# Kernel tuning notes

Hardware: AMD Instinct MI355X
Metric: run time of the kernel (lower is better)

Reference implementation:

```python
import jax, jax.numpy as jnp
import numpy as np

N_EMBD = 1024
N_HEAD = 16
B, T = 2, 2048
EPS_LN = 1e-5
EPS_RENORM = 1e-8


def _layernorm(x, w, b):
    mu = jnp.mean(x, axis=-1, keepdims=True)
    var = jnp.mean(jnp.square(x - mu), axis=-1, keepdims=True)
    return (x - mu) * jax.lax.rsqrt(var + EPS_LN) * w + b


def setup_inputs() -> dict:
    key = jax.random.key(0)
    ks = jax.random.split(key, 8)
    C = N_EMBD
    s = 0.02
    return {
        "x": jax.random.normal(ks[0], (B, T, C), jnp.float32),
        "ln1_w": jnp.ones((C,), jnp.float32),
        "ln1_b": jnp.zeros((C,), jnp.float32),
        "w_attn": jax.random.normal(ks[1], (C, 3 * C), jnp.float32) * s,
        "b_attn": jnp.zeros((3 * C,), jnp.float32),
        "w_attn_proj": jax.random.normal(ks[2], (C, C), jnp.float32) * s,
        "b_attn_proj": jnp.zeros((C,), jnp.float32),
        "threshold": jnp.full((N_HEAD,), 0.01, jnp.float32),
        "leak": jnp.full((N_HEAD,), 2.0, jnp.float32),
        "steepness": jnp.full((N_HEAD,), 2.0, jnp.float32),
        "ln2_w": jnp.ones((C,), jnp.float32),
        "ln2_b": jnp.zeros((C,), jnp.float32),
        "w_fc": jax.random.normal(ks[3], (C, 4 * C), jnp.float32) * s,
        "b_fc": jnp.zeros((4 * C,), jnp.float32),
        "w_mlp_proj": jax.random.normal(ks[4], (4 * C, C), jnp.float32) * s,
        "b_mlp_proj": jnp.zeros((C,), jnp.float32),
    }


def _ember_block(x, ln1_w, ln1_b, w_attn, b_attn, w_attn_proj, b_attn_proj,
                 threshold, leak, steepness, ln2_w, ln2_b,
                 w_fc, b_fc, w_mlp_proj, b_mlp_proj):
    Bx, Tx, C = x.shape
    H = N_HEAD
    D = C // H

    h = _layernorm(x, ln1_w, ln1_b)
    qkv = h @ w_attn + b_attn                      # [B,T,3C]
    q, k, v = jnp.split(qkv, 3, axis=-1)
    q = q.reshape(Bx, Tx, H, D).transpose(0, 2, 1, 3)  # [B,H,T,D]
    k = k.reshape(Bx, Tx, H, D).transpose(0, 2, 1, 3)
    v = v.reshape(Bx, Tx, H, D).transpose(0, 2, 1, 3)

    att = jnp.einsum('bhqd,bhkd->bhqk', q, k) * (1.0 / np.sqrt(D))
    causal = jnp.tril(jnp.ones((Tx, Tx), bool))
    att = jnp.where(causal[None, None], att, -jnp.inf)
    p = jax.nn.softmax(att, axis=-1)               # [B,H,T,T]

    # per-head LIF gating
    th = (jnp.abs(threshold) * 0.1)[None, :, None, None]
    lk = jax.nn.sigmoid(leak)[None, :, None, None]
    st = jax.nn.softplus(steepness)[None, :, None, None]
    fire = jax.nn.sigmoid(st * (p - th))
    w = fire + lk * (1.0 - fire)
    m = p * w
    m = m / (jnp.sum(m, axis=-1, keepdims=True) + EPS_RENORM)

    y = jnp.einsum('bhqk,bhkd->bhqd', m, v)
    y = y.transpose(0, 2, 1, 3).reshape(Bx, Tx, C)
    y = y @ w_attn_proj + b_attn_proj
    x = x + y

    h2 = _layernorm(x, ln2_w, ln2_b)
    h2 = jax.nn.gelu(h2 @ w_fc + b_fc, approximate=False)
    x = x + (h2 @ w_mlp_proj + b_mlp_proj)
    return x


def reference(x, ln1_w, ln1_b, w_attn, b_attn, w_attn_proj, b_attn_proj,
              threshold, leak, steepness, ln2_w, ln2_b,
              w_fc, b_fc, w_mlp_proj, b_mlp_proj):
    return _ember_block(x, ln1_w, ln1_b, w_attn, b_attn, w_attn_proj, b_attn_proj,
                        threshold, leak, steepness, ln2_w, ln2_b,
                        w_fc, b_fc, w_mlp_proj, b_mlp_proj)
```

## Files before the change

kernel.cpp:

```cpp
#include <hip/hip_runtime.h>
#include <hip/hip_bf16.h>
#include <math.h>

typedef __bf16 bf16_t;
typedef __bf16 bf16x8 __attribute__((ext_vector_type(8)));
typedef __bf16 bf16x4 __attribute__((ext_vector_type(4)));
typedef float  f32x4  __attribute__((ext_vector_type(4)));
typedef unsigned int u32;

static constexpr int C_    = 1024;
static constexpr int NH    = 16;
static constexpr int DH    = 64;
static constexpr int BB    = 2;
static constexpr int TT    = 2048;
static constexpr int MROWS = BB * TT;
static constexpr float LOG2E = 1.4426950408889634f;

__device__ __forceinline__ void gload_lds16(const bf16_t* src, bf16_t* dst) {
  __builtin_amdgcn_global_load_lds(
      (const __attribute__((address_space(1))) u32*)(src),
      (__attribute__((address_space(3))) u32*)(dst),
      16, 0, 0);
}

__device__ __forceinline__ u32 cvt_pk_bf16(float a, float b) {
  u32 r;
  asm("v_cvt_pk_bf16_f32 %0, %1, %2" : "=v"(r) : "v"(a), "v"(b));
  return r;
}

__device__ __forceinline__ float fexp2(float x) {
#if __has_builtin(__builtin_amdgcn_exp2f)
  return __builtin_amdgcn_exp2f(x);
#else
  return exp2f(x);
#endif
}
__device__ __forceinline__ float frcp(float x) {
#if __has_builtin(__builtin_amdgcn_rcpf)
  return __builtin_amdgcn_rcpf(x);
#else
  return 1.0f / x;
#endif
}

__device__ __forceinline__ int sc_to_t(int s, int c) {
  if (s < 32)  return s;
  if (s < 64)  return 32 + (s - 32) * 2 + c;
  if (s < 96)  return 96 + (s - 64) * 3 + c;
  return 192 + (s - 96) * 4 + c;
}

__device__ __forceinline__ void item64_to_uc(int item, int& u, int& c) {
  if (item < 8)       { u = item;               c = 0; }
  else if (item < 24) { int v = item - 8;  u = 8  + (v >> 1); c = v & 1; }
  else if (item < 48) { int v = item - 24; u = 16 + v / 3;    c = v - 3 * (v / 3); }
  else                { int v = item - 48; u = 24 + (v >> 2); c = v & 3; }
}

__global__ __launch_bounds__(256) void ln_bf16(
    const float* __restrict__ x, const float* __restrict__ w,
    const float* __restrict__ b, bf16_t* __restrict__ out)
{
  const int row = blockIdx.x;
  const int tid = threadIdx.x;
  const float4 v = reinterpret_cast<const float4*>(x + (size_t)row * C_)[tid];
  float s  = v.x + v.y + v.z + v.w;
  float s2 = v.x*v.x + v.y*v.y + v.z*v.z + v.w*v.w;
#pragma unroll
  for (int m = 1; m < 64; m <<= 1) { s += __shfl_xor(s, m); s2 += __shfl_xor(s2, m); }
  __shared__ float red[8];
  const int wv = tid >> 6;
  if ((tid & 63) == 0) { red[wv] = s; red[4 + wv] = s2; }
  __syncthreads();
  s  = red[0] + red[1] + red[2] + red[3];
  s2 = red[4] + red[5] + red[6] + red[7];
  const float mu   = s * (1.0f / C_);
  const float rstd = rsqrtf(s2 * (1.0f / C_) - mu * mu + 1e-5f);
  const float4 wv4 = reinterpret_cast<const float4*>(w)[tid];
  const float4 bv4 = reinterpret_cast<const float4*>(b)[tid];
  bf16x4 o;
  o[0] = (bf16_t)((v.x - mu) * rstd * wv4.x + bv4.x);
  o[1] = (bf16_t)((v.y - mu) * rstd * wv4.y + bv4.y);
  o[2] = (bf16_t)((v.z - mu) * rstd * wv4.z + bv4.z);
  o[3] = (bf16_t)((v.w - mu) * rstd * wv4.w + bv4.w);
  *reinterpret_cast<bf16x4*>(out + (size_t)row * C_ + tid * 4) = o;
}

__global__ __launch_bounds__(256) void transpose_w(
    const float* __restrict__ in, bf16_t* __restrict__ out, int K, int N)
{
  __shared__ float tile[32][33];
  const int tx = threadIdx.x & 31, ty = threadIdx.x >> 5;
  const int n0 = blockIdx.x * 32, k0 = blockIdx.y * 32;
#pragma unroll
  for (int i = 0; i < 4; ++i)
    tile[ty + i * 8][tx] = in[(size_t)(k0 + ty + i * 8) * N + n0 + tx];
  __syncthreads();
#pragma unroll
  for (int i = 0; i < 4; ++i)
    out[(size_t)(n0 + ty + i * 8) * K + k0 + tx] = (bf16_t)tile[tx][ty + i * 8];
}

__global__ __launch_bounds__(256) void transpose_v(
    const bf16_t* __restrict__ in, bf16_t* __restrict__ out)
{
  __shared__ bf16_t tile[32][33];
  const int bh = blockIdx.z;
  const bf16_t* src = in  + (size_t)bh * TT * DH;
  bf16_t*       dst = out + (size_t)bh * TT * DH;
  const int tx = threadIdx.x & 31, ty = threadIdx.x >> 5;
  const int t0 = blockIdx.x * 32, d0 = blockIdx.y * 32;
#pragma unroll
  for (int i = 0; i < 4; ++i)
    tile[ty + i * 8][tx] = src[(size_t)(t0 + ty + i * 8) * DH + d0 + tx];
  __syncthreads();
#pragma unroll
  for (int i = 0; i < 4; ++i)
    dst[(size_t)(d0 + ty + i * 8) * TT + t0 + tx] = tile[tx][ty + i * 8];
}

template<int EPI>
__global__ __launch_bounds__(256) void gemm_bf16(
    const bf16_t* __restrict__ A, const bf16_t* __restrict__ Bt,
    const float* __restrict__ bias, const float* __restrict__ resid,
    float* __restrict__ fout, bf16_t* __restrict__ bout0,
    bf16_t* __restrict__ bout1, bf16_t* __restrict__ bout2,
    int M, int N, int K)
{
  constexpr int BM = 128, BN = 128, BK = 64;
  __shared__ bf16_t As[BM * BK];
  __shared__ bf16_t Bs[BN * BK];
  const int tid  = threadIdx.x;
  const int wave = tid >> 6, lane = tid & 63;
  const int r = lane & 15, g = lane >> 4;
  const int wm = wave >> 1, wn = wave & 1;
  const int bm = blockIdx.x, bn = blockIdx.y;

  const bf16_t* Abase = A  + (size_t)bm * BM * K;
  const bf16_t* Bbase = Bt + (size_t)bn * BN * K;

  f32x4 acc[4][4] = {};

  for (int kt = 0; kt < K; kt += BK) {
#pragma unroll
    for (int it = 0; it < 4; ++it) {
      const int c0 = it * 256 + wave * 64;
      const int idx = c0 + lane;
      const int rr = idx >> 3, cc = idx & 7;
      const int gs = cc ^ (rr & 7);
      gload_lds16(Abase + (size_t)rr * K + kt + gs * 8, As + c0 * 8);
    }
#pragma unroll
    for (int it = 0; it < 4; ++it) {
      const int c0 = it * 256 + wave * 64;
      const int idx = c0 + lane;
      const int rr = idx >> 3, cc = idx & 7;
      const int gs = cc ^ (rr & 7);
      gload_lds16(Bbase + (size_t)rr * K + kt + gs * 8, Bs + c0 * 8);
    }
    asm volatile("s_waitcnt vmcnt(0)" ::: "memory");
    __syncthreads();
#pragma unroll
    for (int s = 0; s < 2; ++s) {
      bf16x8 af[4], bfr[4];
#pragma unroll
      for (int mi = 0; mi < 4; ++mi) {
        const int rr = wm * 64 + mi * 16 + r;
        const int ch = (s * 4 + g) ^ (rr & 7);
        af[mi] = *reinterpret_cast<const bf16x8*>(&As[rr * BK + ch * 8]);
      }
#pragma unroll
      for (int ni = 0; ni < 4; ++ni) {
        const int rr = wn * 64 + ni * 16 + r;
        const int ch = (s * 4 + g) ^ (rr & 7);
        bfr[ni] = *reinterpret_cast<const bf16x8*>(&Bs[rr * BK + ch * 8]);
      }
#pragma unroll
      for (int mi = 0; mi < 4; ++mi)
#pragma unroll
        for (int ni = 0; ni < 4; ++ni)
          acc[mi][ni] = __builtin_amdgcn_mfma_f32_16x16x32_bf16(
              af[mi], bfr[ni], acc[mi][ni], 0, 0, 0);
    }
    __syncthreads();
  }

#pragma unroll
  for (int mi = 0; mi < 4; ++mi) {
#pragma unroll
    for (int ni = 0; ni < 4; ++ni) {
      const int grow0 = bm * BM + wm * 64 + mi * 16 + g * 4;
      const int gcol  = bn * BN + wn * 64 + ni * 16 + r;
      const float bv = bias[gcol];
#pragma unroll
      for (int i = 0; i < 4; ++i) {
        const int grow = grow0 + i;
        float v = acc[mi][ni][i] + bv;
        if constexpr (EPI == 0) {
          const int which = gcol >> 10;
          const int c0 = gcol & 1023;
          const int hh = c0 >> 6, dd = c0 & 63;
          const int bb = grow >> 11, t = grow & 2047;
          bf16_t* dst = (which == 0) ? bout0 : (which == 1) ? bout1 : bout2;
          dst[((size_t)(bb * NH + hh) * TT + t) * DH + dd] = (bf16_t)v;
        } else if constexpr (EPI == 1) {
          const size_t o = (size_t)grow * N + gcol;
          fout[o] = v + resid[o];
        } else {
          const float gl = 0.5f * v * (1.0f + erff(v * 0.70710678118654752f));
          bout0[(size_t)grow * N + gcol] = (bf16_t)gl;
        }
      }
    }
  }
}


__global__ __launch_bounds__(256, 4) void attn_p1(
    const bf16_t* __restrict__ Q, const bf16_t* __restrict__ Km,
    float2* __restrict__ mzP)
{
  __shared__ bf16_t Ks[2][64 * 64];
  const int tid = threadIdx.x;
  const int w = tid >> 6, lane = tid & 63;
  const int r = lane & 15, g = lane >> 4;
  const int bid = blockIdx.x;
  const int bh  = (bid & 7) * 4 + ((bid >> 3) & 3);
  int u, c; item64_to_uc(bid >> 5, u, c);
  const int cmax = u >> 3;
  const bool diag = (c == cmax);
  const int nt = diag ? (u & 7) + 1 : 8;
  const int s = 4 * u + w;
  const int row0 = u * 64 + w * 16;
  const int qrow = row0 + r;

  const bf16_t* Qh = Q  + (size_t)bh * TT * DH;
  const bf16_t* Kh = Km + (size_t)bh * TT * DH;
  const float SCL = 0.125f * LOG2E;

  bf16x8 qf[2];
#pragma unroll
  for (int s2 = 0; s2 < 2; ++s2) {
    bf16x8 t = *reinterpret_cast<const bf16x8*>(Qh + (size_t)qrow * DH + s2 * 32 + g * 8);
#pragma unroll
    for (int i = 0; i < 8; ++i) t[i] = (bf16_t)((float)t[i] * SCL);
    qf[s2] = t;
  }

  auto STAGEK = [&](int b, int t8) {
#pragma unroll
    for (int it = 0; it < 2; ++it) {
      const int idx = it * 256 + tid;
      const int rr = idx >> 3, cc = idx & 7, gs = cc ^ (rr & 7);
      gload_lds16(Kh + (size_t)(c * 512 + t8 * 64 + rr) * DH + gs * 8, &Ks[b][idx * 8]);
    }
  };

  float runM = -1e30f, runZ = 0.f;
  STAGEK(0, 0);
  for (int t8 = 0; t8 < nt; ++t8) {
    const int b = t8 & 1;
    asm volatile("s_waitcnt vmcnt(0)" ::: "memory");
    __syncthreads();
    if (t8 + 1 < nt) STAGEK(b ^ 1, t8 + 1);
    f32x4 sfT[4] = {};
#pragma unroll
    for (int s2 = 0; s2 < 2; ++s2) {
      bf16x8 kf[4];
#pragma unroll
      for (int ni = 0; ni < 4; ++ni)
        kf[ni] = *reinterpret_cast<const bf16x8*>(
            &Ks[b][(ni * 16 + r) * 64 + (((s2 << 2) | g) ^ (r & 7)) * 8]);
#pragma unroll
      for (int ni = 0; ni < 4; ++ni)
        sfT[ni] = __builtin_amdgcn_mfma_f32_16x16x32_bf16(kf[ni], qf[s2], sfT[ni], 0, 0, 0);
    }
    const bool dm = diag && (t8 == nt - 1);
    const int kbase = c * 512 + t8 * 64;
    float xv[16];
#pragma unroll
    for (int ni = 0; ni < 4; ++ni)
#pragma unroll
      for (int j = 0; j < 4; ++j) {
        float x = sfT[ni][j];
        if (dm) {
          const int kcol = kbase + ni * 16 + g * 4 + j;
          if (kcol > qrow) x = -1e30f;
        }
        xv[ni * 4 + j] = x;
      }
    float nm = runM;
#pragma unroll
    for (int e = 0; e < 16; ++e) nm = fmaxf(nm, xv[e]);
    float z = runZ * fexp2(runM - nm);
#pragma unroll
    for (int e = 0; e < 16; ++e) z += fexp2(xv[e] - nm);
    runM = nm; runZ = z;
  }
#pragma unroll
  for (int msk = 16; msk < 64; msk <<= 1) {
    const float om = __shfl_xor(runM, msk), oz = __shfl_xor(runZ, msk);
    const float nm = fmaxf(runM, om);
    runZ = runZ * fexp2(runM - nm) + oz * fexp2(om - nm);
    runM = nm;
  }
  if (lane < 16)
    mzP[((size_t)(bh * 128 + s) * 4 + c) * 16 + r] = make_float2(runM, runZ);
}

__global__ __launch_bounds__(256, 4) void attn_p3(
    const bf16_t* __restrict__ Q, const bf16_t* __restrict__ Km,
    const bf16_t* __restrict__ Vt, const float2* __restrict__ mzP,
    bf16_t* __restrict__ Y, uint2* __restrict__ yaccA,
    uint2* __restrict__ yaccB, float* __restrict__ denP,
    const float* __restrict__ thrp, const float* __restrict__ leakp,
    const float* __restrict__ steepp)
{
  __shared__ bf16_t Ks[2][64 * 64];
  __shared__ bf16_t Vs[2][64 * 64];
  __shared__ __align__(16) u32 Ms[4][512];

  const int tid = threadIdx.x;
  const int w = tid >> 6, lane = tid & 63;
  const int r = lane & 15, g = lane >> 4;
  const int bid = blockIdx.x;
  const int bh  = (bid & 7) * 4 + ((bid >> 3) & 3);
  int u, c; item64_to_uc(bid >> 5, u, c);
  const int cmax = u >> 3;
  const bool diag = (c == cmax);
  const int nt = diag ? (u & 7) + 1 : 8;
  const int nch = cmax + 1;
  const int s = 4 * u + w;
  const int row0 = u * 64 + w * 16;
  const int qrow = row0 + r;
  const int hh = bh & (NH - 1), bb = bh >> 4;

  const bf16_t* Qh  = Q  + (size_t)bh * TT * DH;
  const bf16_t* Kh  = Km + (size_t)bh * TT * DH;
  const bf16_t* Vth = Vt + (size_t)bh * TT * DH;

  const float lk  = 1.0f / (1.0f + expf(-leakp[hh]));
  const float ilk = 1.0f - lk;
  const float st  = log1pf(expf(steepp[hh]));
  const float Lst = LOG2E * st;
  const float A0  = Lst * (fabsf(thrp[hh]) * 0.1f);

  float M = -1e30f, Z = 0.f;
  for (int c2 = 0; c2 < nch; ++c2) {
    const float2 mz = mzP[((size_t)(bh * 128 + s) * 4 + c2) * 16 + r];
    const float nm = fmaxf(M, mz.x);
    Z = Z * fexp2(M - nm) + mz.y * fexp2(mz.x - nm);
    M = nm;
  }
  const float rcpZ = frcp(Z);

  const float SCL = 0.125f * LOG2E;
  bf16x8 qf[2];
#pragma unroll
  for (int s2 = 0; s2 < 2; ++s2) {
    bf16x8 t = *reinterpret_cast<const bf16x8*>(Qh + (size_t)qrow * DH + s2 * 32 + g * 8);
#pragma unroll
    for (int i = 0; i < 8; ++i) t[i] = (bf16_t)((float)t[i] * SCL);
    qf[s2] = t;
  }
  bf16x8 ones;
#pragma unroll
  for (int i = 0; i < 8; ++i) ones[i] = (bf16_t)1.0f;

  uint2* MsU2 = reinterpret_cast<uint2*>(&Ms[w][0]);
  uint4* MsU4 = reinterpret_cast<uint4*>(&Ms[w][0]);

  auto STAGE = [&](int b, int t8) {
    const int kbase = c * 512 + t8 * 64;
#pragma unroll
    for (int it = 0; it < 2; ++it) {
      const int idx = it * 256 + tid;
      const int rr = idx >> 3, cc = idx & 7, gs = cc ^ (rr & 7);
      gload_lds16(Kh + (size_t)(kbase + rr) * DH + gs * 8, &Ks[b][idx * 8]);
      gload_lds16(Vth + (size_t)rr * TT + kbase + gs * 8, &Vs[b][idx * 8]);
    }
  };

  f32x4 yacc[4] = {};
  f32x4 dacc = {};

  STAGE(0, 0);
  for (int t8 = 0; t8 < nt; ++t8) {
    const int b = t8 & 1;
    asm volatile("s_waitcnt vmcnt(0)" ::: "memory");
    __syncthreads();
    if (t8 + 1 < nt) STAGE(b ^ 1, t8 + 1);
    const int kbase = c * 512 + t8 * 64;
    f32x4 sfT[4] = {};
#pragma unroll
    for (int s2 = 0; s2 < 2; ++s2) {
      bf16x8 kf[4];
#pragma unroll
      for (int ni = 0; ni < 4; ++ni)
        kf[ni] = *reinterpret_cast<const bf16x8*>(
            &Ks[b][(ni * 16 + r) * 64 + (((s2 << 2) | g) ^ (r & 7)) * 8]);
#pragma unroll
      for (int ni = 0; ni < 4; ++ni)
        sfT[ni] = __builtin_amdgcn_mfma_f32_16x16x32_bf16(kf[ni], qf[s2], sfT[ni], 0, 0, 0);
    }
    const bool dm = diag && (t8 == nt - 1);
#pragma unroll
    for (int ni = 0; ni < 4; ++ni) {
      float mv[4];
#pragma unroll
      for (int j = 0; j < 4; ++j) {
        float x = sfT[ni][j];
        if (dm) {
          const int kcol = kbase + ni * 16 + g * 4 + j;
          if (kcol > qrow) x = -1e30f;
        }
        const float p    = fexp2(x - M) * rcpZ;
        const float fire = frcp(1.0f + fexp2(A0 - Lst * p));
        mv[j] = p * fmaf(ilk, fire, lk);
      }
      MsU2[r * 16 + ((4 * ni + g) ^ ((r & 7) << 1))] =
          make_uint2(cvt_pk_bf16(mv[0], mv[1]), cvt_pk_bf16(mv[2], mv[3]));
    }
#pragma unroll
    for (int s2 = 0; s2 < 2; ++s2) {
      const uint4 aw = MsU4[r * 8 + ((s2 * 4 + g) ^ (r & 7))];
      const bf16x8 af = __builtin_bit_cast(bf16x8, aw);
      bf16x8 vf[4];
#pragma unroll
      for (int ni = 0; ni < 4; ++ni)
        vf[ni] = *reinterpret_cast<const bf16x8*>(
            &Vs[b][(ni * 16 + r) * 64 + (((s2 << 2) | g) ^ (r & 7)) * 8]);
#pragma unroll
      for (int ni = 0; ni < 4; ++ni)
        yacc[ni] = __builtin_amdgcn_mfma_f32_16x16x32_bf16(af, vf[ni], yacc[ni], 0, 0, 0);
      dacc = __builtin_amdgcn_mfma_f32_16x16x32_bf16(af, ones, dacc, 0, 0, 0);
    }
  }

  if (nch == 1) {
#pragma unroll
    for (int j = 0; j < 4; ++j) {
      const float rd = frcp(dacc[j] + 1e-8f);
      const int t = row0 + g * 4 + j;
#pragma unroll
      for (int ni = 0; ni < 4; ++ni)
        Y[((size_t)(bb * TT + t)) * C_ + hh * DH + ni * 16 + r] =
            (bf16_t)(yacc[ni][j] * rd);
    }
  } else {
    const int pid = bh * 288 + (sc_to_t(s, c) - 32);
    uint2* pb = (pid < 4096) ? (yaccA + (size_t)pid * 256)
                             : (yaccB + (size_t)(pid - 4096) * 256);
#pragma unroll
    for (int ni = 0; ni < 4; ++ni)
      pb[ni * 64 + lane] =
          make_uint2(cvt_pk_bf16(yacc[ni][0], yacc[ni][1]),
                     cvt_pk_bf16(yacc[ni][2], yacc[ni][3]));
    if (r == 0)
      *reinterpret_cast<float4*>(&denP[(size_t)pid * 16 + g * 4]) =
          make_float4(dacc[0], dacc[1], dacc[2], dacc[3]);
  }
}

__global__ __launch_bounds__(256) void attn_p4(
    const uint2* __restrict__ yaccA, const uint2* __restrict__ yaccB,
    const float* __restrict__ denP, bf16_t* __restrict__ Y)
{
  const int bid = blockIdx.x;
  const int bh  = bid / 96;
  const int s   = 32 + (bid - bh * 96);
  const int nch = (s >> 5) + 1;
  const int hh = bh & (NH - 1), bb = bh >> 4;

  const int tid = threadIdx.x;
  const int w = tid >> 6, lane = tid & 63;
  const int r = lane & 15, g = lane >> 4;

  float acc[4] = {};
  float den[4] = {};
  for (int c = 0; c < nch; ++c) {
    const int pid = bh * 288 + (sc_to_t(s, c) - 32);
    const uint2* pb = (pid < 4096) ? (yaccA + (size_t)pid * 256)
                                   : (yaccB + (size_t)(pid - 4096) * 256);
    const uint2 u = pb[w * 64 + lane];
    acc[0] += __builtin_bit_cast(float, (u.x & 0xFFFFu) << 16);
    acc[1] += __builtin_bit_cast(float, (u.x & 0xFFFF0000u));
    acc[2] += __builtin_bit_cast(float, (u.y & 0xFFFFu) << 16);
    acc[3] += __builtin_bit_cast(float, (u.y & 0xFFFF0000u));
    const float4 d4 = *reinterpret_cast<const float4*>(&denP[(size_t)pid * 16 + g * 4]);
    den[0] += d4.x; den[1] += d4.y; den[2] += d4.z; den[3] += d4.w;
  }
#pragma unroll
  for (int j = 0; j < 4; ++j) {
    const float rd = 1.0f / (den[j] + 1e-8f);
    const int t = s * 16 + g * 4 + j;
    Y[((size_t)(bb * TT + t)) * C_ + hh * DH + w * 16 + r] = (bf16_t)(acc[j] * rd);
  }
}

extern "C" void kernel_launch(void* const* d_in, const int* in_sizes, int n_in,
                              void* d_out, int out_size, void* d_ws, size_t ws_size,
                              hipStream_t stream)
{
  const float* x      = (const float*)d_in[0];
  const float* ln1_w  = (const float*)d_in[1];
  const float* ln1_b  = (const float*)d_in[2];
  const float* w_attn = (const float*)d_in[3];
  const float* b_attn = (const float*)d_in[4];
  const float* w_proj = (const float*)d_in[5];
  const float* b_proj = (const float*)d_in[6];
  const float* thr    = (const float*)d_in[7];
  const float* leak   = (const float*)d_in[8];
  const float* steep  = (const float*)d_in[9];
  const float* ln2_w  = (const float*)d_in[10];
  const float* ln2_b  = (const float*)d_in[11];
  const float* w_fc   = (const float*)d_in[12];
  const float* b_fc   = (const float*)d_in[13];
  const float* w_mlp  = (const float*)d_in[14];
  const float* b_mlp  = (const float*)d_in[15];

  char* ws = (char*)d_ws;
  bf16_t* q    = (bf16_t*)(ws + 0);
  bf16_t* k    = (bf16_t*)(ws + 8388608);
  bf16_t* v    = (bf16_t*)(ws + 16777216);
  bf16_t* vT   = (bf16_t*)(ws + 25165824);
  bf16_t* gbuf = (bf16_t*)(ws + 0);
  bf16_t* hbuf = (bf16_t*)(ws + 33554432);
  float*  x2   = (float*) (ws + 41943040);
  bf16_t* wT_attn = (bf16_t*)(ws + 58720256);
  bf16_t* wT_proj = (bf16_t*)(ws + 65011712);
  bf16_t* wT_fc   = (bf16_t*)(ws + 67108864);
  bf16_t* wT_mlp  = (bf16_t*)(ws + 75497472);

  uint2* yaccA = (uint2*)(ws + 16777216);
  uint2* yaccB = (uint2*)(ws + 41943040);
  float* denP  = (float*)(ws + 52428800);
  float2* mzP  = (float2*)(ws + 53477376);

  float* out = (float*)d_out;

  ln_bf16<<<dim3(MROWS), dim3(256), 0, stream>>>(x, ln1_w, ln1_b, hbuf);
  transpose_w<<<dim3(96, 32),  dim3(256), 0, stream>>>(w_attn, wT_attn, 1024, 3072);
  transpose_w<<<dim3(32, 32),  dim3(256), 0, stream>>>(w_proj, wT_proj, 1024, 1024);
  transpose_w<<<dim3(128, 32), dim3(256), 0, stream>>>(w_fc,   wT_fc,   1024, 4096);
  transpose_w<<<dim3(32, 128), dim3(256), 0, stream>>>(w_mlp,  wT_mlp,  4096, 1024);

  gemm_bf16<0><<<dim3(32, 24), dim3(256), 0, stream>>>(
      hbuf, wT_attn, b_attn, nullptr, nullptr, q, k, v, MROWS, 3072, 1024);
  transpose_v<<<dim3(64, 2, 32), dim3(256), 0, stream>>>(v, vT);

  attn_p1<<<dim3(2560), dim3(256), 0, stream>>>(q, k, mzP);
  attn_p3<<<dim3(2560), dim3(256), 0, stream>>>(
      q, k, vT, mzP, hbuf, yaccA, yaccB, denP, thr, leak, steep);
  attn_p4<<<dim3(3072), dim3(256), 0, stream>>>(yaccA, yaccB, denP, hbuf);

  gemm_bf16<1><<<dim3(32, 8), dim3(256), 0, stream>>>(
      hbuf, wT_proj, b_proj, x, x2, nullptr, nullptr, nullptr, MROWS, 1024, 1024);

  ln_bf16<<<dim3(MROWS), dim3(256), 0, stream>>>(x2, ln2_w, ln2_b, hbuf);

  gemm_bf16<2><<<dim3(32, 32), dim3(256), 0, stream>>>(
      hbuf, wT_fc, b_fc, nullptr, nullptr, gbuf, nullptr, nullptr, MROWS, 4096, 1024);

  gemm_bf16<1><<<dim3(32, 8), dim3(256), 0, stream>>>(
      gbuf, wT_mlp, b_mlp, x2, out, nullptr, nullptr, nullptr, MROWS, 1024, 4096);
}
```

Baseline: 302.0 us.

## Split-K the attention and MLP output projections, fusing partial reduction into LN2

The two N=1024 GEMMs (attention projection and MLP down-projection) now split their K dimension across blockIdx.z, 2-way and 4-way, so each launch has more blocks than the previous 256. Partial sums go to fp32 for the first slice and bf16 for the rest, in reused workspace regions. A new ln2_fuse kernel sums the attention partials, bias and residual, writes x2 and applies LayerNorm in one pass. A combine3 kernel reduces the MLP partials with bias and residual. The cost is extra partial-buffer traffic, an extra combine launch, and bf16 rounding of the partial sums.

```diff
diff --git a/kernel.cpp b/kernel.cpp
--- a/kernel.cpp
+++ b/kernel.cpp
@@ -87,6 +87,68 @@
   *reinterpret_cast<bf16x4*>(out + (size_t)row * C_ + tid * 4) = o;
 }
 
+__global__ __launch_bounds__(256) void ln2_fuse(
+    const float* __restrict__ p0, const bf16_t* __restrict__ p1,
+    const float* __restrict__ xin, const float* __restrict__ pbias,
+    const float* __restrict__ w, const float* __restrict__ b,
+    float* __restrict__ x2out, bf16_t* __restrict__ out)
+{
+  const int row = blockIdx.x;
+  const int tid = threadIdx.x;
+  const size_t base = (size_t)row * C_ + tid * 4;
+  const float4 v0 = *reinterpret_cast<const float4*>(p0 + base);
+  const bf16x4 v1 = *reinterpret_cast<const bf16x4*>(p1 + base);
+  const float4 xr = *reinterpret_cast<const float4*>(xin + base);
+  const float4 pb = *reinterpret_cast<const float4*>(pbias + tid * 4);
+  float4 v;
+  v.x = v0.x + (float)v1[0] + pb.x + xr.x;
+  v.y = v0.y + (float)v1[1] + pb.y + xr.y;
+  v.z = v0.z + (float)v1[2] + pb.z + xr.z;
+  v.w = v0.w + (float)v1[3] + pb.w + xr.w;
+  *reinterpret_cast<float4*>(x2out + base) = v;
+
+  float s  = v.x + v.y + v.z + v.w;
+  float s2 = v.x*v.x + v.y*v.y + v.z*v.z + v.w*v.w;
+#pragma unroll
+  for (int m = 1; m < 64; m <<= 1) { s += __shfl_xor(s, m); s2 += __shfl_xor(s2, m); }
+  __shared__ float red[8];
+  const int wv = tid >> 6;
+  if ((tid & 63) == 0) { red[wv] = s; red[4 + wv] = s2; }
+  __syncthreads();
+  s  = red[0] + red[1] + red[2] + red[3];
+  s2 = red[4] + red[5] + red[6] + red[7];
+  const float mu   = s * (1.0f / C_);
+  const float rstd = rsqrtf(s2 * (1.0f / C_) - mu * mu + 1e-5f);
+  const float4 wv4 = reinterpret_cast<const float4*>(w)[tid];
+  const float4 bv4 = reinterpret_cast<const float4*>(b)[tid];
+  bf16x4 o;
+  o[0] = (bf16_t)((v.x - mu) * rstd * wv4.x + bv4.x);
+  o[1] = (bf16_t)((v.y - mu) * rstd * wv4.y + bv4.y);
+  o[2] = (bf16_t)((v.z - mu) * rstd * wv4.z + bv4.z);
+  o[3] = (bf16_t)((v.w - mu) * rstd * wv4.w + bv4.w);
+  *reinterpret_cast<bf16x4*>(out + base) = o;
+}
+
+__global__ __launch_bounds__(256) void combine3(
+    float* __restrict__ out, const bf16_t* __restrict__ p1,
+    const bf16_t* __restrict__ p2, const bf16_t* __restrict__ p3,
+    const float* __restrict__ bias, const float* __restrict__ resid)
+{
+  const size_t idx = ((size_t)blockIdx.x * 256 + threadIdx.x) * 4;
+  float4 o = *reinterpret_cast<const float4*>(out + idx);
+  const bf16x4 a = *reinterpret_cast<const bf16x4*>(p1 + idx);
+  const bf16x4 b = *reinterpret_cast<const bf16x4*>(p2 + idx);
+  const bf16x4 c = *reinterpret_cast<const bf16x4*>(p3 + idx);
+  const float4 r = *reinterpret_cast<const float4*>(resid + idx);
+  const int col = (int)(idx & (C_ - 1));
+  const float4 bv = *reinterpret_cast<const float4*>(bias + col);
+  o.x += (float)a[0] + (float)b[0] + (float)c[0] + bv.x + r.x;
+  o.y += (float)a[1] + (float)b[1] + (float)c[1] + bv.y + r.y;
+  o.z += (float)a[2] + (float)b[2] + (float)c[2] + bv.z + r.z;
+  o.w += (float)a[3] + (float)b[3] + (float)c[3] + bv.w + r.w;
+  *reinterpret_cast<float4*>(out + idx) = o;
+}
+
 __global__ __launch_bounds__(256) void transpose_w(
     const float* __restrict__ in, bf16_t* __restrict__ out, int K, int N)
 {
@@ -126,7 +188,7 @@
     const float* __restrict__ bias, const float* __restrict__ resid,
     float* __restrict__ fout, bf16_t* __restrict__ bout0,
     bf16_t* __restrict__ bout1, bf16_t* __restrict__ bout2,
-    int M, int N, int K)
+    int M, int N, int Kc, int Kfull)
 {
   constexpr int BM = 128, BN = 128, BK = 64;
   __shared__ bf16_t As[BM * BK];
@@ -136,20 +198,22 @@
   const int r = lane & 15, g = lane >> 4;
   const int wm = wave >> 1, wn = wave & 1;
   const int bm = blockIdx.x, bn = blockIdx.y;
-
-  const bf16_t* Abase = A  + (size_t)bm * BM * K;
-  const bf16_t* Bbase = Bt + (size_t)bn * BN * K;
+  const int z  = blockIdx.z;
+  const int kstart = z * Kc;
+
+  const bf16_t* Abase = A  + (size_t)bm * BM * Kfull;
+  const bf16_t* Bbase = Bt + (size_t)bn * BN * Kfull;
 
   f32x4 acc[4][4] = {};
 
-  for (int kt = 0; kt < K; kt += BK) {
+  for (int kt = kstart; kt < kstart + Kc; kt += BK) {
 #pragma unroll
     for (int it = 0; it < 4; ++it) {
       const int c0 = it * 256 + wave * 64;
       const int idx = c0 + lane;
       const int rr = idx >> 3, cc = idx & 7;
       const int gs = cc ^ (rr & 7);
-      gload_lds16(Abase + (size_t)rr * K + kt + gs * 8, As + c0 * 8);
+      gload_lds16(Abase + (size_t)rr * Kfull + kt + gs * 8, As + c0 * 8);
     }
 #pragma unroll
     for (int it = 0; it < 4; ++it) {
@@ -157,7 +221,7 @@
       const int idx = c0 + lane;
       const int rr = idx >> 3, cc = idx & 7;
       const int gs = cc ^ (rr & 7);
-      gload_lds16(Bbase + (size_t)rr * K + kt + gs * 8, Bs + c0 * 8);
+      gload_lds16(Bbase + (size_t)rr * Kfull + kt + gs * 8, Bs + c0 * 8);
     }
     asm volatile("s_waitcnt vmcnt(0)" ::: "memory");
     __syncthreads();
@@ -192,7 +256,7 @@
     for (int ni = 0; ni < 4; ++ni) {
       const int grow0 = bm * BM + wm * 64 + mi * 16 + g * 4;
       const int gcol  = bn * BN + wn * 64 + ni * 16 + r;
-      const float bv = bias[gcol];
+      const float bv = (EPI == 3) ? 0.f : bias[gcol];
 #pragma unroll
       for (int i = 0; i < 4; ++i) {
         const int grow = grow0 + i;
@@ -207,9 +271,16 @@
         } else if constexpr (EPI == 1) {
           const size_t o = (size_t)grow * N + gcol;
           fout[o] = v + resid[o];
-        } else {
+        } else if constexpr (EPI == 2) {
           const float gl = 0.5f * v * (1.0f + erff(v * 0.70710678118654752f));
           bout0[(size_t)grow * N + gcol] = (bf16_t)gl;
+        } else {
+          const size_t o = (size_t)grow * N + gcol;
+          if (z == 0) fout[o] = v;
+          else {
+            bf16_t* pb = (z == 1) ? bout0 : (z == 2) ? bout1 : bout2;
+            pb[o] = (bf16_t)v;
+          }
         }
       }
     }
@@ -538,6 +609,11 @@
   float* denP  = (float*)(ws + 52428800);
   float2* mzP  = (float2*)(ws + 53477376);
 
+  bf16_t* pp1 = (bf16_t*)(ws + 0);
+  bf16_t* mp1 = (bf16_t*)(ws + 33554432);
+  bf16_t* mp2 = (bf16_t*)(ws + 58720256);
+  bf16_t* mp3 = (bf16_t*)(ws + 67108864);
+
   float* out = (float*)d_out;
 
   ln_bf16<<<dim3(MROWS), dim3(256), 0, stream>>>(x, ln1_w, ln1_b, hbuf);
@@ -546,8 +622,8 @@
   transpose_w<<<dim3(128, 32), dim3(256), 0, stream>>>(w_fc,   wT_fc,   1024, 4096);
   transpose_w<<<dim3(32, 128), dim3(256), 0, stream>>>(w_mlp,  wT_mlp,  4096, 1024);
 
-  gemm_bf16<0><<<dim3(32, 24), dim3(256), 0, stream>>>(
-      hbuf, wT_attn, b_attn, nullptr, nullptr, q, k, v, MROWS, 3072, 1024);
+  gemm_bf16<0><<<dim3(32, 24, 1), dim3(256), 0, stream>>>(
+      hbuf, wT_attn, b_attn, nullptr, nullptr, q, k, v, MROWS, 3072, 1024, 1024);
   transpose_v<<<dim3(64, 2, 32), dim3(256), 0, stream>>>(v, vT);
 
   attn_p1<<<dim3(2560), dim3(256), 0, stream>>>(q, k, mzP);
@@ -555,14 +631,20 @@
       q, k, vT, mzP, hbuf, yaccA, yaccB, denP, thr, leak, steep);
   attn_p4<<<dim3(3072), dim3(256), 0, stream>>>(yaccA, yaccB, denP, hbuf);
 
-  gemm_bf16<1><<<dim3(32, 8), dim3(256), 0, stream>>>(
-      hbuf, wT_proj, b_proj, x, x2, nullptr, nullptr, nullptr, MROWS, 1024, 1024);
-
-  ln_bf16<<<dim3(MROWS), dim3(256), 0, stream>>>(x2, ln2_w, ln2_b, hbuf);
-
-  gemm_bf16<2><<<dim3(32, 32), dim3(256), 0, stream>>>(
-      hbuf, wT_fc, b_fc, nullptr, nullptr, gbuf, nullptr, nullptr, MROWS, 4096, 1024);
-
-  gemm_bf16<1><<<dim3(32, 8), dim3(256), 0, stream>>>(
-      gbuf, wT_mlp, b_mlp, x2, out, nullptr, nullptr, nullptr, MROWS, 1024, 4096);
-}
+  gemm_bf16<3><<<dim3(32, 8, 2), dim3(256), 0, stream>>>(
+      hbuf, wT_proj, nullptr, nullptr, x2, pp1, nullptr, nullptr,
+      MROWS, 1024, 512, 1024);
+
+  ln2_fuse<<<dim3(MROWS), dim3(256), 0, stream>>>(
+      x2, pp1, x, b_proj, ln2_w, ln2_b, x2, hbuf);
+
+  gemm_bf16<2><<<dim3(32, 32, 1), dim3(256), 0, stream>>>(
+      hbuf, wT_fc, b_fc, nullptr, nullptr, gbuf, nullptr, nullptr,
+      MROWS, 4096, 1024, 1024);
+
+  gemm_bf16<3><<<dim3(32, 8, 4), dim3(256), 0, stream>>>(
+      gbuf, wT_mlp, nullptr, nullptr, out, mp1, mp2, mp3,
+      MROWS, 1024, 1024, 4096);
+
+  combine3<<<dim3(4096), dim3(256), 0, stream>>>(out, mp1, mp2, mp3, b_mlp, x2);
+}
```

Result: faster. 295.2 us (-2.3%).
